# Kernel tuning notes

Hardware: AMD Instinct MI355X
Metric: run time of the kernel (lower is better)

Reference implementation:

```python
import jax, jax.numpy as jnp
import numpy as np
import math

D = 1024
K = 64
MLP = 4 * D
LN_EPS = 1e-5

def _layernorm(x, g, b):
    mu = jnp.mean(x, axis=-1, keepdims=True)
    var = jnp.var(x, axis=-1, keepdims=True)
    return (x - mu) * jax.lax.rsqrt(var + LN_EPS) * g + b

def setup_inputs() -> dict:
    key = jax.random.key(0)
    ks = jax.random.split(key, 10)
    B, T = 4, 4096
    x = jax.random.normal(ks[0], (B, T, D), dtype=jnp.float32)
    state = jnp.zeros((B, K, 2), dtype=jnp.float32)
    s = 0.02 / math.sqrt(D)
    eigvec_real = jax.random.normal(ks[1], (K, D), dtype=jnp.float32) * s
    eigvec_imag = jax.random.normal(ks[2], (K, D), dtype=jnp.float32) * s
    alpha = jax.random.uniform(ks[3], (K,), minval=-3.0, maxval=0.0, dtype=jnp.float32)
    omega = jnp.linspace(0.0, 2 * math.pi * (1 - 1.0 / K), K, dtype=jnp.float32)
    resonance_eps = jnp.float32(0.01)
    resonance_M = jax.random.normal(ks[4], (K, K), dtype=jnp.float32) / math.sqrt(K)
    out_w = jax.random.normal(ks[5], (D, D), dtype=jnp.float32) * 0.02
    out_b = jnp.zeros((D,), dtype=jnp.float32)
    w1 = jax.random.normal(ks[6], (D, MLP), dtype=jnp.float32) * 0.02
    b1 = jnp.zeros((MLP,), dtype=jnp.float32)
    w2 = jax.random.normal(ks[7], (MLP, D), dtype=jnp.float32) * 0.02
    b2 = jnp.zeros((D,), dtype=jnp.float32)
    g1 = jnp.ones((D,), dtype=jnp.float32); be1 = jnp.zeros((D,), dtype=jnp.float32)
    g2 = jnp.ones((D,), dtype=jnp.float32); be2 = jnp.zeros((D,), dtype=jnp.float32)
    return {"x": x, "state": state, "eigvec_real": eigvec_real, "eigvec_imag": eigvec_imag,
            "alpha": alpha, "omega": omega, "resonance_eps": resonance_eps,
            "resonance_M": resonance_M, "out_w": out_w, "out_b": out_b,
            "w1": w1, "b1": b1, "w2": w2, "b2": b2,
            "g1": g1, "be1": be1, "g2": g2, "be2": be2}

def reference(x, state, eigvec_real, eigvec_imag, alpha, omega, resonance_eps,
              resonance_M, out_w, out_b, w1, b1, w2, b2, g1, be1, g2, be2):
    B, T, _ = x.shape
    residual = x
    xn = _layernorm(x, g1, be1)
    # eigenvalues with |lambda| <= 1
    mag = jax.nn.sigmoid(alpha)
    lam_r = mag * jnp.cos(omega)   # (K,)
    lam_i = mag * jnp.sin(omega)
    R = jnp.eye(K, dtype=x.dtype) + resonance_eps * resonance_M  # (K,K)
    # projection onto eigenvectors
    beta_r = jnp.einsum('btd,kd->btk', xn, eigvec_real)
    beta_i = jnp.einsum('btd,kd->btk', xn, -eigvec_imag)
    c_r0 = state[:, :, 0]
    c_i0 = state[:, :, 1]
    Rt = R.T  # for bj @ Rt == einsum('kj,bj->bk', R, c)

    def step(carry, b):
        cr, ci = carry
        br, bi = b
        ncr = lam_r * cr - lam_i * ci + br
        nci = lam_r * ci + lam_i * cr + bi
        return (ncr, nci), (ncr @ Rt, nci @ Rt)

    (c_r, c_i), (ys_r, ys_i) = jax.lax.scan(
        step, (c_r0, c_i0),
        (jnp.swapaxes(beta_r, 0, 1), jnp.swapaxes(beta_i, 0, 1)))
    c_seq_r = jnp.swapaxes(ys_r, 0, 1)  # (B,T,K)
    c_seq_i = jnp.swapaxes(ys_i, 0, 1)
    h = jnp.einsum('btk,kd->btd', c_seq_r, eigvec_real) - jnp.einsum('btk,kd->btd', c_seq_i, eigvec_imag)
    h = h @ out_w + out_b
    y = residual + h
    yn = _layernorm(y, g2, be2)
    mlp_out = jax.nn.gelu(yn @ w1 + b1, approximate=False) @ w2 + b2
    out = y + mlp_out
    final_state = jnp.stack([c_r, c_i], axis=-1)
    return out, final_state
```

## Files before the change

### kernel.cpp

```cpp
#include <hip/hip_runtime.h>
#include <hip/hip_bf16.h>
#include <math.h>


#define D 1024
#define TSEQ 4096
#define BT_ROWS 16384
#define CHUNK 4096

typedef __attribute__((ext_vector_type(8))) _Float16 f16x8;
typedef __attribute__((ext_vector_type(4))) _Float16 f16x4;
typedef __attribute__((ext_vector_type(4))) float f32x4;

__device__ inline _Float16 f2h(float f) { return (_Float16)f; }

#define GLL16(g, l)                                                              \
  __builtin_amdgcn_global_load_lds(                                              \
      (const __attribute__((address_space(1))) void*)(g),                        \
      (__attribute__((address_space(3))) void*)(l), 16, 0, 0)

template <int EPI, int NFRAG>
__global__ __launch_bounds__(256) void gemm_bt(
    const _Float16* __restrict__ A, const _Float16* __restrict__ Bt,
    int N, int Kd,
    float* __restrict__ Cf, _Float16* __restrict__ Ch,
    const float* __restrict__ bias, const float* __restrict__ resid)
{
  constexpr int BN = NFRAG * 32;
  constexpr int BCALLS = BN / 32;
  constexpr int ASZ = 128 * 64;
  constexpr int BSZ = BN * 64;
  __shared__ __align__(16) _Float16 lds[2][ASZ + BSZ];

  const int t = threadIdx.x;
  const int wid = t >> 6, lane = t & 63;
  const int brow = blockIdx.y << 7;
  const int bcol = blockIdx.x * BN;
  const int wr = wid >> 1, wc = wid & 1;

  f32x4 acc[4][NFRAG] = {};

  const int srow = t >> 3;
  const int skb = (((t & 7) ^ (srow & 7)) << 3);
  const _Float16* gA = A + (size_t)(brow + srow) * Kd + skb;
  const _Float16* gB = Bt + (size_t)(bcol + srow) * Kd + skb;

  const int rr = lane & 15, g = lane >> 4;

  auto stage = [&](int buf, int k0) {
    _Float16* dst = &lds[buf][0];
#pragma unroll
    for (int i = 0; i < 4; ++i)
      GLL16(gA + (size_t)(i * 32) * Kd + k0, dst + i * 2048 + t * 8);
#pragma unroll
    for (int i = 0; i < BCALLS; ++i)
      GLL16(gB + (size_t)(i * 32) * Kd + k0, dst + ASZ + i * 2048 + t * 8);
  };

  const int nsteps = Kd >> 6;
  stage(0, 0);
  int cur = 0;
  for (int s = 0; s < nsteps; ++s) {
    if (s + 1 < nsteps) {
      stage(cur ^ 1, (s + 1) << 6);
      if constexpr (NFRAG == 4) asm volatile("s_waitcnt vmcnt(8)" ::: "memory");
      else                      asm volatile("s_waitcnt vmcnt(6)" ::: "memory");
    } else {
      asm volatile("s_waitcnt vmcnt(0)" ::: "memory");
    }
    __builtin_amdgcn_s_barrier();

    const _Float16* la = &lds[cur][0];
    const _Float16* lb = la + ASZ;
#pragma unroll
    for (int kk = 0; kk < 2; ++kk) {
      f16x8 af[4], bfr[NFRAG];
#pragma unroll
      for (int m = 0; m < 4; ++m) {
        const int row = wr * 64 + m * 16 + rr;
        af[m] = *(const f16x8*)&la[row * 64 + (((g + 4 * kk) ^ (row & 7)) << 3)];
      }
#pragma unroll
      for (int n = 0; n < NFRAG; ++n) {
        const int row = wc * (BN / 2) + n * 16 + rr;
        bfr[n] = *(const f16x8*)&lb[row * 64 + (((g + 4 * kk) ^ (row & 7)) << 3)];
      }
#pragma unroll
      for (int m = 0; m < 4; ++m)
#pragma unroll
        for (int n = 0; n < NFRAG; ++n)
          acc[m][n] = __builtin_amdgcn_mfma_f32_16x16x32_f16(af[m], bfr[n], acc[m][n], 0, 0, 0);
    }
    asm volatile("s_waitcnt lgkmcnt(0)" ::: "memory");
    __builtin_amdgcn_s_barrier();
    cur ^= 1;
  }

  const int cc = lane & 15;
  const int rb = (lane >> 4) << 2;
#pragma unroll
  for (int m = 0; m < 4; ++m) {
#pragma unroll
    for (int n = 0; n < NFRAG; ++n) {
      const int gr = brow + wr * 64 + m * 16 + rb;
      const int gc = bcol + wc * (BN / 2) + n * 16 + cc;
#pragma unroll
      for (int q = 0; q < 4; ++q) {
        const size_t idx = (size_t)(gr + q) * N + gc;
        const float v = acc[m][n][q];
        if constexpr (EPI == 0) {
          Cf[idx] = v;
        } else if constexpr (EPI == 1) {
          Cf[idx] = resid[idx] + v + bias[gc];
        } else {
          const float u = v + bias[gc];
          Ch[idx] = f2h(0.5f * u * (1.0f + erff(u * 0.70710678118654752f)));
        }
      }
    }
  }
}

__global__ __launch_bounds__(256) void ln_f16(
    const float* __restrict__ x, const float* __restrict__ g,
    const float* __restrict__ b, _Float16* __restrict__ out)
{
  const int row = blockIdx.x;
  const int t = threadIdx.x;
  const size_t base = (size_t)row * D + t * 4;
  const float4 v = *(const float4*)(x + base);
  float s = v.x + v.y + v.z + v.w;
  float q = v.x * v.x + v.y * v.y + v.z * v.z + v.w * v.w;
#pragma unroll
  for (int off = 32; off > 0; off >>= 1) {
    s += __shfl_xor(s, off);
    q += __shfl_xor(q, off);
  }
  __shared__ float rs[4], rq[4];
  const int wid = t >> 6, lane = t & 63;
  if (lane == 0) { rs[wid] = s; rq[wid] = q; }
  __syncthreads();
  s = rs[0] + rs[1] + rs[2] + rs[3];
  q = rq[0] + rq[1] + rq[2] + rq[3];
  const float mean = s * (1.0f / D);
  const float var = q * (1.0f / D) - mean * mean;
  const float rstd = rsqrtf(var + 1e-5f);
  const float4 gg = *(const float4*)(g + t * 4);
  const float4 bb = *(const float4*)(b + t * 4);
  f16x4 o;
  o[0] = f2h((v.x - mean) * rstd * gg.x + bb.x);
  o[1] = f2h((v.y - mean) * rstd * gg.y + bb.y);
  o[2] = f2h((v.z - mean) * rstd * gg.z + bb.z);
  o[3] = f2h((v.w - mean) * rstd * gg.w + bb.w);
  *(f16x4*)(out + base) = o;
}

__global__ __launch_bounds__(64) void scan_k(
    const float* __restrict__ beta, const float* __restrict__ state,
    const float* __restrict__ alpha, const float* __restrict__ omega,
    _Float16* __restrict__ c_cat, float* __restrict__ fs)
{
  const int k = threadIdx.x;
  const int chunk = blockIdx.x;
  const int b = blockIdx.y;
  const float a = alpha[k];
  const float mag = 1.0f / (1.0f + expf(-a));
  const float om = omega[k];
  const float lr = mag * cosf(om);
  const float li = mag * sinf(om);
  const int t0 = chunk * 64;
  float cr, ci;
  int t;
  if (chunk == 0) {
    cr = state[(b * 64 + k) * 2 + 0];
    ci = state[(b * 64 + k) * 2 + 1];
    t = 0;
  } else {
    cr = 0.0f; ci = 0.0f;
    t = t0 - 64;
  }
  for (; t < t0 + 64; ++t) {
    const float* bp = beta + ((size_t)(b * TSEQ + t) << 7);
    const float br = bp[k];
    const float bi = bp[64 + k];
    const float ncr = lr * cr - li * ci + br;
    const float nci = lr * ci + li * cr + bi;
    cr = ncr; ci = nci;
    if (t >= t0) {
      _Float16* cp = c_cat + ((size_t)(b * TSEQ + t) << 7);
      cp[k] = f2h(cr);
      cp[64 + k] = f2h(ci);
    }
  }
  if (chunk == 63) {
    fs[(b * 64 + k) * 2 + 0] = cr;
    fs[(b * 64 + k) * 2 + 1] = ci;
  }
}

__global__ void tr_cvt(const float* __restrict__ src, _Float16* __restrict__ dst,
                       int R, int C)
{
  __shared__ float tile[32][33];
  const int bx = blockIdx.x * 32;
  const int by = blockIdx.y * 32;
  const int tx = threadIdx.x, ty = threadIdx.y;
#pragma unroll
  for (int i = 0; i < 32; i += 8)
    tile[ty + i][tx] = src[(size_t)(by + ty + i) * C + bx + tx];
  __syncthreads();
#pragma unroll
  for (int i = 0; i < 32; i += 8)
    dst[(size_t)(bx + ty + i) * R + by + tx] = f2h(tile[tx][ty + i]);
}

__global__ void build_Ecat(const float* __restrict__ er, const float* __restrict__ ei,
                           _Float16* __restrict__ E)
{
  const int i = blockIdx.x * 256 + threadIdx.x;
  const float v = (i < 65536) ? er[i] : -ei[i - 65536];
  E[i] = f2h(v);
}

__global__ void build_G(const float* __restrict__ er, const float* __restrict__ ei,
                        const float* __restrict__ Mm, const float* __restrict__ epsp,
                        float* __restrict__ G)
{
  const int j = blockIdx.y;
  const int d = blockIdx.x * 256 + threadIdx.x;
  const float* e = (j < 64) ? er : ei;
  const int jj = j & 63;
  const float eps = epsp[0];
  float acc = 0.0f;
  for (int k = 0; k < 64; ++k)
    acc += Mm[k * 64 + jj] * e[(size_t)k * D + d];
  const float v = e[(size_t)jj * D + d] + eps * acc;
  G[(size_t)j * D + d] = (j < 64) ? v : -v;
}

__global__ void build_WhoT(const float* __restrict__ G, const float* __restrict__ ow,
                           _Float16* __restrict__ WhoT)
{
  const int j = blockIdx.y;
  const int d = blockIdx.x * 256 + threadIdx.x;
  float acc = 0.0f;
  for (int k = 0; k < D; ++k)
    acc += G[(size_t)j * D + k] * ow[(size_t)k * D + d];
  WhoT[(size_t)d * 128 + j] = f2h(acc);
}

extern "C" void kernel_launch(void* const* d_in, const int* in_sizes, int n_in,
                              void* d_out, int out_size, void* d_ws, size_t ws_size,
                              hipStream_t stream) {
  const float* x     = (const float*)d_in[0];
  const float* state = (const float*)d_in[1];
  const float* er    = (const float*)d_in[2];
  const float* ei    = (const float*)d_in[3];
  const float* alpha = (const float*)d_in[4];
  const float* omega = (const float*)d_in[5];
  const float* epsv  = (const float*)d_in[6];
  const float* Mm    = (const float*)d_in[7];
  const float* out_w = (const float*)d_in[8];
  const float* out_b = (const float*)d_in[9];
  const float* w1    = (const float*)d_in[10];
  const float* b1    = (const float*)d_in[11];
  const float* w2    = (const float*)d_in[12];
  const float* b2    = (const float*)d_in[13];
  const float* g1    = (const float*)d_in[14];
  const float* be1   = (const float*)d_in[15];
  const float* g2    = (const float*)d_in[16];
  const float* be2   = (const float*)d_in[17];

  float* out = (float*)d_out;
  float* fs  = out + (size_t)BT_ROWS * D;
  float* y   = out;

  char* w = (char*)d_ws;
  _Float16* act  = (_Float16*)(w);
  float*    beta = (float*)   (w);
  _Float16* ccat = (_Float16*)(w + 8388608u);
  _Float16* xnyn = (_Float16*)(w + 33554432u);
  _Float16* w1T  = (_Float16*)(w + 67108864u);
  _Float16* w2T  = (_Float16*)(w + 75497472u);
  float*    G    = (float*)   (w + 83886080u);
  _Float16* WhoT = (_Float16*)(w + 84410368u);
  _Float16* Ecat = (_Float16*)(w + 84672512u);

  build_Ecat<<<512, 256, 0, stream>>>(er, ei, Ecat);
  build_G<<<dim3(4, 128), 256, 0, stream>>>(er, ei, Mm, epsv, G);
  build_WhoT<<<dim3(4, 128), 256, 0, stream>>>(G, out_w, WhoT);
  tr_cvt<<<dim3(128, 32), dim3(32, 8), 0, stream>>>(w1, w1T, 1024, 4096);
  tr_cvt<<<dim3(32, 128), dim3(32, 8), 0, stream>>>(w2, w2T, 4096, 1024);

  ln_f16<<<BT_ROWS, 256, 0, stream>>>(x, g1, be1, xnyn);
  gemm_bt<0, 2><<<dim3(2, 128), 256, 0, stream>>>(xnyn, Ecat, 128, 1024, beta, nullptr, nullptr, nullptr);
  scan_k<<<dim3(64, 4), 64, 0, stream>>>(beta, state, alpha, omega, ccat, fs);

  gemm_bt<1, 4><<<dim3(8, 128), 256, 0, stream>>>(ccat, WhoT, 1024, 128, y, nullptr, out_b, x);
  ln_f16<<<BT_ROWS, 256, 0, stream>>>(y, g2, be2, xnyn);

  for (int c = 0; c < BT_ROWS / CHUNK; ++c) {
    const size_t ro = (size_t)c * CHUNK;
    gemm_bt<2, 4><<<dim3(32, CHUNK / 128), 256, 0, stream>>>(
        xnyn + ro * D, w1T, 4096, 1024, nullptr, act, b1, nullptr);
    gemm_bt<1, 2><<<dim3(16, CHUNK / 128), 256, 0, stream>>>(
        act, w2T, 1024, 4096, out + ro * D, nullptr, b2, y + ro * D);
  }
}
```

Measured before the change: 710.9 us.

## Add 256x256-tile eight-wave GEMM with interleaved staging for the MLP up-projection

Adds a new GEMM kernel with a 256x256 output tile, 512 threads and 128 KB of dynamic LDS. It stages half-tiles of the next K-slice between four MFMA phases, with barriers and s_setprio around the MFMA bursts. The first MLP GEMM (with the bias+GELU epilogue) now uses this kernel instead of the 128x128 tile kernel. The aim is more operand reuse per byte loaded and better overlap of global-to-LDS loads with matrix math. In exchange, the large LDS footprint limits residency to about one block per CU and makes register pressure high.

```diff
diff --git a/kernel.cpp b/kernel.cpp
--- a/kernel.cpp
+++ b/kernel.cpp
@@ -18,6 +18,160 @@
   __builtin_amdgcn_global_load_lds(                                              \
       (const __attribute__((address_space(1))) void*)(g),                        \
       (__attribute__((address_space(3))) void*)(l), 16, 0, 0)
+
+#define WAITVM(n)  asm volatile("s_waitcnt vmcnt(" #n ")" ::: "memory")
+#define WAITLGKM() asm volatile("s_waitcnt lgkmcnt(0)" ::: "memory")
+
+template <int EPI>
+__global__ __launch_bounds__(512, 2) void gemm256(
+    const _Float16* __restrict__ A, const _Float16* __restrict__ Bt,
+    int N, int Kd,
+    float* __restrict__ Cf, _Float16* __restrict__ Ch,
+    const float* __restrict__ bias, const float* __restrict__ resid)
+{
+  extern __shared__ __align__(16) _Float16 ldsraw[];
+  const int t = threadIdx.x;
+  const int wid = t >> 6, lane = t & 63;
+  const int wr = wid >> 2, wc = wid & 3;
+  const int brow = blockIdx.y << 8, bcol = blockIdx.x << 8;
+
+  f32x4 acc[8][4] = {};
+
+  const int srow = t >> 3;
+  const int skb8 = ((t & 7) ^ (srow & 7)) << 3;
+  const _Float16* gA = A + (size_t)(brow + srow) * Kd + skb8;
+  const _Float16* gB = Bt + (size_t)(bcol + srow) * Kd + skb8;
+  const int ldst = t * 8;
+
+  auto stageH = [&](int buf, int obase, int h, int kt) {
+    const _Float16* gp = obase ? gB : gA;
+    _Float16* dst = ldsraw + buf * 32768 + obase + h * 8192 + ldst;
+    GLL16(gp + (size_t)(h * 128) * Kd + (size_t)kt * 64, dst);
+    GLL16(gp + (size_t)(h * 128 + 64) * Kd + (size_t)kt * 64, dst + 4096);
+  };
+
+  const int rr = lane & 15, g4 = lane >> 4;
+  auto rdA = [&](int buf, int m, int kk) -> f16x8 {
+    const int row = wr * 128 + m * 16 + rr;
+    const int kblk = kk * 4 + g4;
+    return *(const f16x8*)&ldsraw[buf * 32768 + row * 64 + ((kblk ^ (row & 7)) << 3)];
+  };
+  auto rdB = [&](int buf, int n, int kk) -> f16x8 {
+    const int row = wc * 64 + n * 16 + rr;
+    const int kblk = kk * 4 + g4;
+    return *(const f16x8*)&ldsraw[buf * 32768 + 16384 + row * 64 + ((kblk ^ (row & 7)) << 3)];
+  };
+
+  const int nt = Kd >> 6;
+
+  stageH(0, 0, 0, 0); stageH(0, 0, 1, 0);
+  stageH(0, 16384, 0, 0); stageH(0, 16384, 1, 0);
+  stageH(1, 0, 0, 1);
+  WAITVM(2);
+  __builtin_amdgcn_s_barrier();
+
+  f16x8 af[4][2], bf0[2][2], bf1[2][2];
+
+  for (int j = 0; j < nt; ++j) {
+    const int c = j & 1;
+
+    if (j + 1 < nt) stageH(c ^ 1, 0, 1, j + 1);
+#pragma unroll
+    for (int m = 0; m < 4; ++m)
+#pragma unroll
+      for (int kk = 0; kk < 2; ++kk) af[m][kk] = rdA(c, m, kk);
+#pragma unroll
+    for (int n = 0; n < 2; ++n)
+#pragma unroll
+      for (int kk = 0; kk < 2; ++kk) bf0[n][kk] = rdB(c, n, kk);
+    WAITLGKM();
+    __builtin_amdgcn_s_setprio(1);
+#pragma unroll
+    for (int m = 0; m < 4; ++m)
+#pragma unroll
+      for (int n = 0; n < 2; ++n)
+#pragma unroll
+        for (int kk = 0; kk < 2; ++kk)
+          acc[m][n] = __builtin_amdgcn_mfma_f32_16x16x32_f16(af[m][kk], bf0[n][kk], acc[m][n], 0, 0, 0);
+    __builtin_amdgcn_s_setprio(0);
+    __builtin_amdgcn_s_barrier();
+
+    if (j + 1 < nt) stageH(c ^ 1, 16384, 0, j + 1);
+#pragma unroll
+    for (int n = 0; n < 2; ++n)
+#pragma unroll
+      for (int kk = 0; kk < 2; ++kk) bf1[n][kk] = rdB(c, n + 2, kk);
+    WAITLGKM();
+    __builtin_amdgcn_s_setprio(1);
+#pragma unroll
+    for (int m = 0; m < 4; ++m)
+#pragma unroll
+      for (int n = 0; n < 2; ++n)
+#pragma unroll
+        for (int kk = 0; kk < 2; ++kk)
+          acc[m][n + 2] = __builtin_amdgcn_mfma_f32_16x16x32_f16(af[m][kk], bf1[n][kk], acc[m][n + 2], 0, 0, 0);
+    __builtin_amdgcn_s_setprio(0);
+    __builtin_amdgcn_s_barrier();
+
+    if (j + 1 < nt) stageH(c ^ 1, 16384, 1, j + 1);
+#pragma unroll
+    for (int m = 0; m < 4; ++m)
+#pragma unroll
+      for (int kk = 0; kk < 2; ++kk) af[m][kk] = rdA(c, m + 4, kk);
+    WAITLGKM();
+    __builtin_amdgcn_s_setprio(1);
+#pragma unroll
+    for (int m = 0; m < 4; ++m)
+#pragma unroll
+      for (int n = 0; n < 2; ++n)
+#pragma unroll
+        for (int kk = 0; kk < 2; ++kk)
+          acc[m + 4][n] = __builtin_amdgcn_mfma_f32_16x16x32_f16(af[m][kk], bf0[n][kk], acc[m + 4][n], 0, 0, 0);
+    __builtin_amdgcn_s_setprio(0);
+    __builtin_amdgcn_s_barrier();
+
+    if (j + 2 < nt) stageH(c, 0, 0, j + 2);
+    __builtin_amdgcn_s_setprio(1);
+#pragma unroll
+    for (int m = 0; m < 4; ++m)
+#pragma unroll
+      for (int n = 0; n < 2; ++n)
+#pragma unroll
+        for (int kk = 0; kk < 2; ++kk)
+          acc[m + 4][n + 2] = __builtin_amdgcn_mfma_f32_16x16x32_f16(af[m][kk], bf1[n][kk], acc[m + 4][n + 2], 0, 0, 0);
+    __builtin_amdgcn_s_setprio(0);
+
+    if (j + 1 < nt) {
+      if (j + 2 < nt) { WAITVM(2); }
+      else            { WAITVM(0); }
+      __builtin_amdgcn_s_barrier();
+    }
+  }
+
+  const int cc = lane & 15;
+  const int rb = (lane >> 4) << 2;
+#pragma unroll
+  for (int m = 0; m < 8; ++m) {
+#pragma unroll
+    for (int n = 0; n < 4; ++n) {
+      const int gr = brow + wr * 128 + m * 16 + rb;
+      const int gc = bcol + wc * 64 + n * 16 + cc;
+#pragma unroll
+      for (int q = 0; q < 4; ++q) {
+        const size_t idx = (size_t)(gr + q) * N + gc;
+        const float v = acc[m][n][q];
+        if constexpr (EPI == 0) {
+          Cf[idx] = v;
+        } else if constexpr (EPI == 1) {
+          Cf[idx] = resid[idx] + v + bias[gc];
+        } else {
+          const float u = v + bias[gc];
+          Ch[idx] = f2h(0.5f * u * (1.0f + erff(u * 0.70710678118654752f)));
+        }
+      }
+    }
+  }
+}
 
 template <int EPI, int NFRAG>
 __global__ __launch_bounds__(256) void gemm_bt(
@@ -63,10 +217,10 @@
   for (int s = 0; s < nsteps; ++s) {
     if (s + 1 < nsteps) {
       stage(cur ^ 1, (s + 1) << 6);
-      if constexpr (NFRAG == 4) asm volatile("s_waitcnt vmcnt(8)" ::: "memory");
-      else                      asm volatile("s_waitcnt vmcnt(6)" ::: "memory");
+      if constexpr (NFRAG == 4) { WAITVM(8); }
+      else                      { WAITVM(6); }
     } else {
-      asm volatile("s_waitcnt vmcnt(0)" ::: "memory");
+      WAITVM(0);
     }
     __builtin_amdgcn_s_barrier();
 
@@ -91,7 +245,7 @@
         for (int n = 0; n < NFRAG; ++n)
           acc[m][n] = __builtin_amdgcn_mfma_f32_16x16x32_f16(af[m], bfr[n], acc[m][n], 0, 0, 0);
     }
-    asm volatile("s_waitcnt lgkmcnt(0)" ::: "memory");
+    WAITLGKM();
     __builtin_amdgcn_s_barrier();
     cur ^= 1;
   }
@@ -301,7 +455,7 @@
 
   for (int c = 0; c < BT_ROWS / CHUNK; ++c) {
     const size_t ro = (size_t)c * CHUNK;
-    gemm_bt<2, 4><<<dim3(32, CHUNK / 128), 256, 0, stream>>>(
+    gemm256<2><<<dim3(16, CHUNK / 256), 512, 131072, stream>>>(
         xnyn + ro * D, w1T, 4096, 1024, nullptr, act, b1, nullptr);
     gemm_bt<1, 2><<<dim3(16, CHUNK / 128), 256, 0, stream>>>(
         act, w2T, 1024, 4096, out + ro * D, nullptr, b2, y + ro * D);
```

Result: faster. 689.8 us (-3.0%).
